# Optimization experiments

Hardware: AMD Instinct MI355X
Metric: run time of the kernel (lower is better)

## Reference

```python
import jax, jax.numpy as jnp
import numpy as np

# ---- Cl(4,1) algebra tables (metric: e1..e4 square to +1, e5 to -1) ----
_METRIC = [1.0, 1.0, 1.0, 1.0, -1.0]

def _popcount(x):
    return bin(x).count('1')

def _gp_blade(a, b):
    # geometric product of basis blades given as bitmasks -> (result_mask, sign)
    s = 1.0
    aa = a >> 1
    swaps = 0
    while aa:
        swaps += _popcount(aa & b)
        aa >>= 1
    if swaps & 1:
        s = -s
    for i in range(5):
        if (a & b) & (1 << i):
            s *= _METRIC[i]
    return a ^ b, s

def _build_gp_map():
    # lane ordering: blades sorted by (grade, bitmask) -> lane 0 scalar, 1..5 vectors, ...
    masks = sorted(range(32), key=lambda m: (_popcount(m), m))
    idx = {m: i for i, m in enumerate(masks)}
    gp = np.zeros((32, 32, 32), dtype=np.float32)
    for a in range(32):
        for b in range(32):
            r, s = _gp_blade(masks[a], masks[b])
            gp[a, b, idx[r]] = s
    return gp

_GP_NP = _build_gp_map()
# signature: scalar part of blade*blade (metric sign per lane)
_SIG_NP = np.array([_GP_NP[k, k, 0] for k in range(32)], dtype=np.float32)

N_HEADS = 8
EPS = 1e-6

def normalize_cl41(x):
    # normalize each 32-lane multivector to unit Euclidean magnitude
    n = jnp.sqrt(jnp.sum(x * x, axis=-1, keepdims=True) + EPS)
    return x / n

def versor_linear(x, w, gp):
    # x: (B,S,I,32), w: (O,I,32), gp: (32,32,32)
    w_op = jnp.einsum('oij,jlk->oilk', w, gp)          # (O,I,32,32)
    out = jnp.einsum('bsil,oilk->bsok', x, w_op)       # (B,S,O,32)
    return normalize_cl41(out)

def setup_inputs() -> dict:
    key = jax.random.key(0)
    ks = jax.random.split(key, 5)
    B, S, D = 2, 2048, 64
    std = 1.0 / (D * 32) ** 0.5
    x = jax.random.normal(ks[0], (B, S, D, 32), dtype=jnp.float32)
    wq = jax.random.normal(ks[1], (D, D, 32), dtype=jnp.float32) * std
    wk = jax.random.normal(ks[2], (D, D, 32), dtype=jnp.float32) * std
    wv = jax.random.normal(ks[3], (D, D, 32), dtype=jnp.float32) * std
    wo = jax.random.normal(ks[4], (D, D, 32), dtype=jnp.float32) * std
    return {'x': x, 'wq': wq, 'wk': wk, 'wv': wv, 'wo': wo}

def reference(x, wq, wk, wv, wo):
    gp = jnp.asarray(_GP_NP)
    sig = jnp.asarray(_SIG_NP)
    B, S, D, _ = x.shape
    H = N_HEADS
    hd = D // H
    def split_heads(t):
        return t.reshape(B, S, H, hd, 32).transpose(0, 2, 1, 3, 4)  # (B,H,S,hd,32)
    q = split_heads(versor_linear(x, wq, gp))
    k = split_heads(versor_linear(x, wk, gp))
    v = split_heads(versor_linear(x, wv, gp))
    q_flat = (q * sig).reshape(B, H, S, hd * 32)
    k_flat = k.reshape(B, H, S, hd * 32)
    score = jnp.einsum('bhqf,bhkf->bhqk', q_flat, k_flat) / (hd ** 0.5)
    attn = jax.nn.softmax(score, axis=-1)
    out = jnp.einsum('bhsi,bhidl->bhsdl', attn, v)      # (B,H,S,hd,32)
    out = out.transpose(0, 2, 1, 3, 4).reshape(B, S, D, 32)
    return versor_linear(out, wo, gp)
```

## Files before the change

### kernel.cpp

```cpp
#include <hip/hip_runtime.h>
#include <hip/hip_bf16.h>


typedef unsigned short u16;
typedef unsigned short u16x8 __attribute__((ext_vector_type(8)));
typedef unsigned short u16x4 __attribute__((ext_vector_type(4)));
typedef short          s16x8 __attribute__((ext_vector_type(8)));
typedef float          f32x4 __attribute__((ext_vector_type(4)));

#define B_DIM 2
#define S_DIM 2048
#define D_DIM 64
#define NH    8
#define HD    256
#define F_DIM 2048
#define TOK   4096

__constant__ int LANE_MASK[32] = {
    0,
    1, 2, 4, 8, 16,
    3, 5, 6, 9, 10, 12, 17, 18, 20, 24,
    7, 11, 13, 14, 19, 21, 22, 25, 26, 28,
    15, 23, 27, 29, 30,
    31};
__constant__ int MASK_LANE[32] = {
    0, 1, 2, 6, 3, 7, 8, 16, 4, 9, 10, 17, 11, 18, 19, 26,
    5, 12, 13, 20, 14, 21, 22, 27, 15, 23, 24, 28, 25, 29, 30, 31};

__device__ __forceinline__ float gp_sign(int a, int b) {
  int swaps = 0;
  int aa = a >> 1;
  while (aa) { swaps += __popc(aa & b); aa >>= 1; }
  float s = (swaps & 1) ? -1.0f : 1.0f;
  if (a & b & 16) s = -s;
  return s;
}

__device__ __forceinline__ u16 f2bf(float f) {
  unsigned u = __float_as_uint(f);
  u += 0x7fffu + ((u >> 16) & 1u);
  return (u16)(u >> 16);
}

__device__ __forceinline__ f32x4 mfma16(s16x8 a, s16x8 b, f32x4 c) {
  return __builtin_amdgcn_mfma_f32_16x16x32_bf16(a, b, c, 0, 0, 0);
}

__device__ __forceinline__ void gload16(const u16* g, u16* l) {
  __builtin_amdgcn_global_load_lds(
      (const __attribute__((address_space(1))) void*)g,
      (__attribute__((address_space(3))) void*)l, 16, 0, 0);
}

__global__ __launch_bounds__(256) void k_cast(const float* __restrict__ x,
                                              u16* __restrict__ xb) {
  int i = blockIdx.x * 256 + threadIdx.x;
  const float4* x4 = (const float4*)x;
  float4 a = x4[2 * i], b = x4[2 * i + 1];
  u16x8 r;
  r[0] = f2bf(a.x); r[1] = f2bf(a.y); r[2] = f2bf(a.z); r[3] = f2bf(a.w);
  r[4] = f2bf(b.x); r[5] = f2bf(b.y); r[6] = f2bf(b.z); r[7] = f2bf(b.w);
  *(u16x8*)&xb[8 * i] = r;
}

__global__ __launch_bounds__(256) void k_buildw(const float* __restrict__ w,
                                                u16* __restrict__ W) {
  __shared__ float wvals[32];
  __shared__ int   jt[1024];
  __shared__ float st[1024];
  const int o = blockIdx.x >> 6, i = blockIdx.x & 63;
  const int tid = threadIdx.x;
  for (int e = tid; e < 1024; e += 256) {
    int k = e >> 5, l = e & 31;
    int mk = LANE_MASK[k], ml = LANE_MASK[l];
    int mj = mk ^ ml;
    jt[e] = MASK_LANE[mj];
    st[e] = gp_sign(mj, ml);
  }
  if (tid < 32) wvals[tid] = w[(o * D_DIM + i) * 32 + tid];
  __syncthreads();
  for (int e = tid; e < 1024; e += 256) {
    int k = e >> 5, l = e & 31;
    size_t off = (size_t)(o * 32 + k) * F_DIM + i * 32 + l;
    W[off] = f2bf(st[e] * wvals[jt[e]]);
  }
}

__global__ __launch_bounds__(256) void k_gemm_qkv(const u16* __restrict__ A,
                                                  const u16* __restrict__ Wcat,
                                                  u16* __restrict__ Qb,
                                                  u16* __restrict__ Kb,
                                                  u16* __restrict__ Vt) {
  constexpr int K = F_DIM;
  __shared__ u16 As[128 * 64];
  __shared__ u16 Bs[128 * 64];
  const int tid = threadIdx.x;
  const int wid = tid >> 6, lane = tid & 63;
  const int region = blockIdx.x >> 4;
  const int col0 = (blockIdx.x & 15) * 128;
  const int row0 = blockIdx.y * 128;
  const u16* Bsrc = Wcat + (size_t)region * F_DIM * F_DIM;
  const int wm = (wid >> 1) * 64, wn = (wid & 1) * 64;
  const int lr = lane & 15, lk = (lane >> 4) * 8;
  const int srow = lane >> 3, scol = (lane & 7) * 8;

  f32x4 acc[4][4];
#pragma unroll
  for (int m = 0; m < 4; ++m)
#pragma unroll
    for (int n = 0; n < 4; ++n) acc[m][n] = (f32x4)0.0f;

  for (int k0 = 0; k0 < K; k0 += 64) {
#pragma unroll
    for (int it = 0; it < 4; ++it) {
      int c = it * 4 + wid;
      gload16(&A[(size_t)(row0 + c * 8 + srow) * K + k0 + scol], &As[c * 512]);
      gload16(&Bsrc[(size_t)(col0 + c * 8 + srow) * K + k0 + scol], &Bs[c * 512]);
    }
    __syncthreads();
#pragma unroll
    for (int ks = 0; ks < 64; ks += 32) {
      s16x8 af[4], bf[4];
#pragma unroll
      for (int m = 0; m < 4; ++m)
        af[m] = *(const s16x8*)&As[(wm + m * 16 + lr) * 64 + ks + lk];
#pragma unroll
      for (int n = 0; n < 4; ++n)
        bf[n] = *(const s16x8*)&Bs[(wn + n * 16 + lr) * 64 + ks + lk];
#pragma unroll
      for (int m = 0; m < 4; ++m)
#pragma unroll
        for (int n = 0; n < 4; ++n)
          acc[m][n] = mfma16(af[m], bf[n], acc[m][n]);
    }
    __syncthreads();
  }

  float sc0 = 1.0f, sc1 = 1.0f;
  if (region == 0) {
    const float qs = 0.35355339059327373f * 1.4426950408889634f;
    int m0 = LANE_MASK[lr], m1 = LANE_MASK[16 + lr];
    sc0 = gp_sign(m0, m0) * qs;
    sc1 = gp_sign(m1, m1) * qs;
  }
#pragma unroll
  for (int m = 0; m < 4; ++m) {
    int rowb = row0 + wm + m * 16 + (lane >> 4) * 4;
#pragma unroll
    for (int np = 0; np < 2; ++np) {
      int n0 = 2 * np, n1 = n0 + 1;
      int colb = col0 + wn + np * 32 + lr;
      f32x4 inv;
#pragma unroll
      for (int r = 0; r < 4; ++r) {
        float a0 = acc[m][n0][r], a1 = acc[m][n1][r];
        float s2 = a0 * a0 + a1 * a1;
        s2 += __shfl_xor(s2, 1);
        s2 += __shfl_xor(s2, 2);
        s2 += __shfl_xor(s2, 4);
        s2 += __shfl_xor(s2, 8);
        inv[r] = 1.0f / sqrtf(s2 + 1e-6f);
      }
      if (region == 2) {
        int bb = rowb >> 11, s0 = rowb & 2047;
        u16x4 p0, p1;
#pragma unroll
        for (int r = 0; r < 4; ++r) {
          p0[r] = f2bf(acc[m][n0][r] * inv[r]);
          p1[r] = f2bf(acc[m][n1][r] * inv[r]);
        }
        *(u16x4*)&Vt[((size_t)bb * F_DIM + colb) * S_DIM + s0] = p0;
        *(u16x4*)&Vt[((size_t)bb * F_DIM + colb + 16) * S_DIM + s0] = p1;
      } else {
        u16* dst = (region == 0) ? Qb : Kb;
#pragma unroll
        for (int r = 0; r < 4; ++r) {
          size_t o = (size_t)(rowb + r) * F_DIM + colb;
          dst[o]      = f2bf(acc[m][n0][r] * inv[r] * sc0);
          dst[o + 16] = f2bf(acc[m][n1][r] * inv[r] * sc1);
        }
      }
    }
  }
}

__global__ __launch_bounds__(256) void k_gemm_fin(const u16* __restrict__ A,
                                                  const u16* __restrict__ B,
                                                  float* __restrict__ outf) {
  constexpr int K = F_DIM, N = F_DIM;
  __shared__ u16 As[128 * 64];
  __shared__ u16 Bs[128 * 64];
  const int tid = threadIdx.x;
  const int wid = tid >> 6, lane = tid & 63;
  const int row0 = blockIdx.y * 128, col0 = blockIdx.x * 128;
  const int wm = (wid >> 1) * 64, wn = (wid & 1) * 64;
  const int lr = lane & 15, lk = (lane >> 4) * 8;
  const int srow = lane >> 3, scol = (lane & 7) * 8;

  f32x4 acc[4][4];
#pragma unroll
  for (int m = 0; m < 4; ++m)
#pragma unroll
    for (int n = 0; n < 4; ++n) acc[m][n] = (f32x4)0.0f;

  for (int k0 = 0; k0 < K; k0 += 64) {
#pragma unroll
    for (int it = 0; it < 4; ++it) {
      int c = it * 4 + wid;
      gload16(&A[(size_t)(row0 + c * 8 + srow) * K + k0 + scol], &As[c * 512]);
      gload16(&B[(size_t)(col0 + c * 8 + srow) * K + k0 + scol], &Bs[c * 512]);
    }
    __syncthreads();
#pragma unroll
    for (int ks = 0; ks < 64; ks += 32) {
      s16x8 af[4], bf[4];
#pragma unroll
      for (int m = 0; m < 4; ++m)
        af[m] = *(const s16x8*)&As[(wm + m * 16 + lr) * 64 + ks + lk];
#pragma unroll
      for (int n = 0; n < 4; ++n)
        bf[n] = *(const s16x8*)&Bs[(wn + n * 16 + lr) * 64 + ks + lk];
#pragma unroll
      for (int m = 0; m < 4; ++m)
#pragma unroll
        for (int n = 0; n < 4; ++n)
          acc[m][n] = mfma16(af[m], bf[n], acc[m][n]);
    }
    __syncthreads();
  }

#pragma unroll
  for (int m = 0; m < 4; ++m) {
    int rowb = row0 + wm + m * 16 + (lane >> 4) * 4;
#pragma unroll
    for (int np = 0; np < 2; ++np) {
      int n0 = 2 * np, n1 = n0 + 1;
      int colb = col0 + wn + np * 32 + lr;
#pragma unroll
      for (int r = 0; r < 4; ++r) {
        float a0 = acc[m][n0][r], a1 = acc[m][n1][r];
        float s2 = a0 * a0 + a1 * a1;
        s2 += __shfl_xor(s2, 1);
        s2 += __shfl_xor(s2, 2);
        s2 += __shfl_xor(s2, 4);
        s2 += __shfl_xor(s2, 8);
        float inv = 1.0f / sqrtf(s2 + 1e-6f);
        size_t o = (size_t)(rowb + r) * N + colb;
        outf[o]      = a0 * inv;
        outf[o + 16] = a1 * inv;
      }
    }
  }
}

__global__ __launch_bounds__(512, 2) void k_attn(const u16* __restrict__ qb,
                                                 const u16* __restrict__ kb,
                                                 const u16* __restrict__ vt,
                                                 u16* __restrict__ ao) {
  __shared__ u16 Kbuf[2][64 * 256];
  __shared__ u16 Vbuf[2][256 * 64];
  __shared__ u16 Ps[8][16][72];
  const int tid = threadIdx.x, wid = tid >> 6, lane = tid & 63;
  const int rid = (blockIdx.x & 7) * 32 + (blockIdx.x >> 3);
  const int qblk = rid & 15, bh = rid >> 4;
  const int b = bh >> 3, h = bh & 7;
  const int lr = lane & 15, hi = lane >> 4;
  const int lr7s = (lr & 7) << 3;
  const int q0 = qblk * 128 + wid * 16;

  const int krow_l = lane >> 5;
  const int kcolb  = (lane & 31) * 8;
  const int vrow_l = lane >> 3;
  const int vcol_l = ((lane & 7) * 8) ^ ((vrow_l & 7) << 3);

  u16x8 qf[8];
#pragma unroll
  for (int c = 0; c < 8; ++c)
    qf[c] = *(const u16x8*)&qb[(size_t)(b * S_DIM + q0 + lr) * F_DIM +
                               h * HD + c * 32 + hi * 8];

  float mrow[4], lacc[4];
#pragma unroll
  for (int r = 0; r < 4; ++r) { mrow[r] = -1e30f; lacc[r] = 0.0f; }
  f32x4 oacc[16];
#pragma unroll
  for (int d = 0; d < 16; ++d) oacc[d] = (f32x4)0.0f;

  const u16* kbase = kb + (size_t)b * S_DIM * F_DIM + h * HD;
  const u16* vbase = vt + ((size_t)b * F_DIM + h * HD) * S_DIM;

#pragma unroll
  for (int i = 0; i < 4; ++i) {
    int ck = wid * 4 + i;
    int kr = ck * 2 + krow_l;
    gload16(kbase + (size_t)kr * F_DIM + (kcolb ^ ((kr & 7) << 3)),
            &Kbuf[0][ck * 512]);
    int vr = ck * 8 + vrow_l;
    gload16(vbase + (size_t)vr * S_DIM + vcol_l, &Vbuf[0][ck * 512]);
  }
  __syncthreads();

  for (int t = 0; t < 32; ++t) {
    const int cur = t & 1;
    if (t < 31) {
      int kv1 = (t + 1) * 64;
#pragma unroll
      for (int i = 0; i < 4; ++i) {
        int ck = wid * 4 + i;
        int kr = ck * 2 + krow_l;
        gload16(kbase + (size_t)(kv1 + kr) * F_DIM + (kcolb ^ ((kr & 7) << 3)),
                &Kbuf[cur ^ 1][ck * 512]);
        int vr = ck * 8 + vrow_l;
        gload16(vbase + (size_t)vr * S_DIM + kv1 + vcol_l,
                &Vbuf[cur ^ 1][ck * 512]);
      }
    }

    f32x4 sacc[4];
#pragma unroll
    for (int n = 0; n < 4; ++n) sacc[n] = (f32x4)0.0f;
#pragma unroll
    for (int c = 0; c < 8; ++c) {
      s16x8 a = *(const s16x8*)&qf[c];
#pragma unroll
      for (int n = 0; n < 4; ++n) {
        s16x8 kf = *(const s16x8*)&Kbuf[cur][(n * 16 + lr) * 256 +
                                             ((c * 32 + hi * 8) ^ lr7s)];
        sacc[n] = mfma16(a, kf, sacc[n]);
      }
    }

    float pmax[4], need = 0.0f;
#pragma unroll
    for (int r = 0; r < 4; ++r) {
      float mx = fmaxf(fmaxf(sacc[0][r], sacc[1][r]),
                       fmaxf(sacc[2][r], sacc[3][r]));
      mx = fmaxf(mx, __shfl_xor(mx, 1));
      mx = fmaxf(mx, __shfl_xor(mx, 2));
      mx = fmaxf(mx, __shfl_xor(mx, 4));
      mx = fmaxf(mx, __shfl_xor(mx, 8));
      pmax[r] = mx;
      need = fmaxf(need, mx - mrow[r]);
    }
    if (!__all(need <= 8.0f)) {
#pragma unroll
      for (int r = 0; r < 4; ++r) {
        float mnew = fmaxf(mrow[r], pmax[r]);
        float alpha = exp2f(mrow[r] - mnew);
        mrow[r] = mnew;
        lacc[r] *= alpha;
#pragma unroll
        for (int d = 0; d < 16; ++d) oacc[d][r] *= alpha;
      }
    }
#pragma unroll
    for (int n = 0; n < 4; ++n)
#pragma unroll
      for (int r = 0; r < 4; ++r) {
        float p = exp2f(sacc[n][r] - mrow[r]);
        lacc[r] += p;
        Ps[wid][hi * 4 + r][n * 16 + lr] = f2bf(p);
      }

#pragma unroll
    for (int ks = 0; ks < 2; ++ks) {
      s16x8 pf = *(const s16x8*)&Ps[wid][lr][ks * 32 + hi * 8];
#pragma unroll
      for (int d0 = 0; d0 < 16; ++d0) {
        s16x8 vf = *(const s16x8*)&Vbuf[cur][(d0 * 16 + lr) * 64 +
                                             ((ks * 32 + hi * 8) ^ lr7s)];
        oacc[d0] = mfma16(pf, vf, oacc[d0]);
      }
    }
    __syncthreads();
  }

#pragma unroll
  for (int r = 0; r < 4; ++r) {
    float s = lacc[r];
    s += __shfl_xor(s, 1);
    s += __shfl_xor(s, 2);
    s += __shfl_xor(s, 4);
    s += __shfl_xor(s, 8);
    float inv = 1.0f / s;
    int row = q0 + hi * 4 + r;
#pragma unroll
    for (int d0 = 0; d0 < 16; ++d0)
      ao[(size_t)(b * S_DIM + row) * F_DIM + h * HD + d0 * 16 + lr] =
          f2bf(oacc[d0][r] * inv);
  }
}

extern "C" void kernel_launch(void* const* d_in, const int* in_sizes, int n_in,
                              void* d_out, int out_size, void* d_ws, size_t ws_size,
                              hipStream_t stream) {
  const float* x  = (const float*)d_in[0];
  const float* wq = (const float*)d_in[1];
  const float* wk = (const float*)d_in[2];
  const float* wv = (const float*)d_in[3];
  const float* wo = (const float*)d_in[4];

  char* ws = (char*)d_ws;
  const size_t SZ_XB = (size_t)TOK * F_DIM * sizeof(u16);
  const size_t SZ_W  = (size_t)F_DIM * F_DIM * sizeof(u16);
  u16* Xb   = (u16*)(ws);
  u16* Wcat = (u16*)(ws + SZ_XB);
  u16* Qb   = (u16*)(ws + SZ_XB + 3 * SZ_W);
  u16* Kb   = Qb + (size_t)TOK * F_DIM;
  u16* Vt   = (u16*)d_out;
  u16* Ao   = Xb;

  const int bw_blocks = D_DIM * D_DIM;

  k_cast<<<TOK * F_DIM / (256 * 8), 256, 0, stream>>>(x, Xb);

  k_buildw<<<bw_blocks, 256, 0, stream>>>(wq, Wcat);
  k_buildw<<<bw_blocks, 256, 0, stream>>>(wk, Wcat + (size_t)F_DIM * F_DIM);
  k_buildw<<<bw_blocks, 256, 0, stream>>>(wv, Wcat + 2 * (size_t)F_DIM * F_DIM);

  k_gemm_qkv<<<dim3(48, 32), 256, 0, stream>>>(Xb, Wcat, Qb, Kb, Vt);

  k_attn<<<B_DIM * NH * (S_DIM / 128), 512, 0, stream>>>(Qb, Kb, Vt, Ao);

  k_buildw<<<bw_blocks, 256, 0, stream>>>(wo, Wcat);
  k_gemm_fin<<<dim3(16, 32), 256, 0, stream>>>(Ao, Wcat, (float*)d_out);
}
```

Measured before the change: 443.3 us.

## Double-buffer LDS tiles in GEMMs and fuse weight-expansion launches

Both bf16 GEMM kernels now use two LDS buffers per operand. The next K-tile's global-to-LDS loads are issued before computing on the current tile, so memory latency overlaps the MFMA work. The four separate weight-expansion launches become one kernel that writes all four expanded matrices, with the output weights in their own workspace slot instead of being rebuilt after attention. The cost is double the LDS per GEMM block, which lowers occupancy, plus an extra weight matrix of workspace.

```diff
diff --git a/kernel.cpp b/kernel.cpp
--- a/kernel.cpp
+++ b/kernel.cpp
@@ -63,13 +63,17 @@
   *(u16x8*)&xb[8 * i] = r;
 }
 
-__global__ __launch_bounds__(256) void k_buildw(const float* __restrict__ w,
-                                                u16* __restrict__ W) {
-  __shared__ float wvals[32];
+__global__ __launch_bounds__(256) void k_buildw4(const float* __restrict__ wq,
+                                                 const float* __restrict__ wk,
+                                                 const float* __restrict__ wv,
+                                                 const float* __restrict__ wo,
+                                                 u16* __restrict__ W) {
+  __shared__ float wvals[4][32];
   __shared__ int   jt[1024];
   __shared__ float st[1024];
   const int o = blockIdx.x >> 6, i = blockIdx.x & 63;
   const int tid = threadIdx.x;
+  constexpr size_t WSZ = (size_t)F_DIM * F_DIM;
   for (int e = tid; e < 1024; e += 256) {
     int k = e >> 5, l = e & 31;
     int mk = LANE_MASK[k], ml = LANE_MASK[l];
@@ -77,12 +81,23 @@
     jt[e] = MASK_LANE[mj];
     st[e] = gp_sign(mj, ml);
   }
-  if (tid < 32) wvals[tid] = w[(o * D_DIM + i) * 32 + tid];
+  if (tid < 32) {
+    int base = (o * D_DIM + i) * 32 + tid;
+    wvals[0][tid] = wq[base];
+    wvals[1][tid] = wk[base];
+    wvals[2][tid] = wv[base];
+    wvals[3][tid] = wo[base];
+  }
   __syncthreads();
   for (int e = tid; e < 1024; e += 256) {
     int k = e >> 5, l = e & 31;
     size_t off = (size_t)(o * 32 + k) * F_DIM + i * 32 + l;
-    W[off] = f2bf(st[e] * wvals[jt[e]]);
+    float s = st[e];
+    int   j = jt[e];
+    W[off]           = f2bf(s * wvals[0][j]);
+    W[off + WSZ]     = f2bf(s * wvals[1][j]);
+    W[off + 2 * WSZ] = f2bf(s * wvals[2][j]);
+    W[off + 3 * WSZ] = f2bf(s * wvals[3][j]);
   }
 }
 
@@ -92,8 +107,8 @@
                                                   u16* __restrict__ Kb,
                                                   u16* __restrict__ Vt) {
   constexpr int K = F_DIM;
-  __shared__ u16 As[128 * 64];
-  __shared__ u16 Bs[128 * 64];
+  __shared__ u16 As[2][128 * 64];
+  __shared__ u16 Bs[2][128 * 64];
   const int tid = threadIdx.x;
   const int wid = tid >> 6, lane = tid & 63;
   const int region = blockIdx.x >> 4;
@@ -110,23 +125,36 @@
 #pragma unroll
     for (int n = 0; n < 4; ++n) acc[m][n] = (f32x4)0.0f;
 
-  for (int k0 = 0; k0 < K; k0 += 64) {
-#pragma unroll
-    for (int it = 0; it < 4; ++it) {
-      int c = it * 4 + wid;
-      gload16(&A[(size_t)(row0 + c * 8 + srow) * K + k0 + scol], &As[c * 512]);
-      gload16(&Bsrc[(size_t)(col0 + c * 8 + srow) * K + k0 + scol], &Bs[c * 512]);
-    }
-    __syncthreads();
+#pragma unroll
+  for (int it = 0; it < 4; ++it) {
+    int c = it * 4 + wid;
+    gload16(&A[(size_t)(row0 + c * 8 + srow) * K + scol], &As[0][c * 512]);
+    gload16(&Bsrc[(size_t)(col0 + c * 8 + srow) * K + scol], &Bs[0][c * 512]);
+  }
+  __syncthreads();
+
+  for (int kt = 0; kt < K / 64; ++kt) {
+    const int cur = kt & 1;
+    if (kt < K / 64 - 1) {
+      int k1 = (kt + 1) * 64;
+#pragma unroll
+      for (int it = 0; it < 4; ++it) {
+        int c = it * 4 + wid;
+        gload16(&A[(size_t)(row0 + c * 8 + srow) * K + k1 + scol],
+                &As[cur ^ 1][c * 512]);
+        gload16(&Bsrc[(size_t)(col0 + c * 8 + srow) * K + k1 + scol],
+                &Bs[cur ^ 1][c * 512]);
+      }
+    }
 #pragma unroll
     for (int ks = 0; ks < 64; ks += 32) {
       s16x8 af[4], bf[4];
 #pragma unroll
       for (int m = 0; m < 4; ++m)
-        af[m] = *(const s16x8*)&As[(wm + m * 16 + lr) * 64 + ks + lk];
+        af[m] = *(const s16x8*)&As[cur][(wm + m * 16 + lr) * 64 + ks + lk];
 #pragma unroll
       for (int n = 0; n < 4; ++n)
-        bf[n] = *(const s16x8*)&Bs[(wn + n * 16 + lr) * 64 + ks + lk];
+        bf[n] = *(const s16x8*)&Bs[cur][(wn + n * 16 + lr) * 64 + ks + lk];
 #pragma unroll
       for (int m = 0; m < 4; ++m)
 #pragma unroll
@@ -188,8 +216,8 @@
                                                   const u16* __restrict__ B,
                                                   float* __restrict__ outf) {
   constexpr int K = F_DIM, N = F_DIM;
-  __shared__ u16 As[128 * 64];
-  __shared__ u16 Bs[128 * 64];
+  __shared__ u16 As[2][128 * 64];
+  __shared__ u16 Bs[2][128 * 64];
   const int tid = threadIdx.x;
   const int wid = tid >> 6, lane = tid & 63;
   const int row0 = blockIdx.y * 128, col0 = blockIdx.x * 128;
@@ -203,23 +231,36 @@
 #pragma unroll
     for (int n = 0; n < 4; ++n) acc[m][n] = (f32x4)0.0f;
 
-  for (int k0 = 0; k0 < K; k0 += 64) {
-#pragma unroll
-    for (int it = 0; it < 4; ++it) {
-      int c = it * 4 + wid;
-      gload16(&A[(size_t)(row0 + c * 8 + srow) * K + k0 + scol], &As[c * 512]);
-      gload16(&B[(size_t)(col0 + c * 8 + srow) * K + k0 + scol], &Bs[c * 512]);
-    }
-    __syncthreads();
+#pragma unroll
+  for (int it = 0; it < 4; ++it) {
+    int c = it * 4 + wid;
+    gload16(&A[(size_t)(row0 + c * 8 + srow) * K + scol], &As[0][c * 512]);
+    gload16(&B[(size_t)(col0 + c * 8 + srow) * K + scol], &Bs[0][c * 512]);
+  }
+  __syncthreads();
+
+  for (int kt = 0; kt < K / 64; ++kt) {
+    const int cur = kt & 1;
+    if (kt < K / 64 - 1) {
+      int k1 = (kt + 1) * 64;
+#pragma unroll
+      for (int it = 0; it < 4; ++it) {
+        int c = it * 4 + wid;
+        gload16(&A[(size_t)(row0 + c * 8 + srow) * K + k1 + scol],
+                &As[cur ^ 1][c * 512]);
+        gload16(&B[(size_t)(col0 + c * 8 + srow) * K + k1 + scol],
+                &Bs[cur ^ 1][c * 512]);
+      }
+    }
 #pragma unroll
     for (int ks = 0; ks < 64; ks += 32) {
       s16x8 af[4], bf[4];
 #pragma unroll
       for (int m = 0; m < 4; ++m)
-        af[m] = *(const s16x8*)&As[(wm + m * 16 + lr) * 64 + ks + lk];
+        af[m] = *(const s16x8*)&As[cur][(wm + m * 16 + lr) * 64 + ks + lk];
 #pragma unroll
       for (int n = 0; n < 4; ++n)
-        bf[n] = *(const s16x8*)&Bs[(wn + n * 16 + lr) * 64 + ks + lk];
+        bf[n] = *(const s16x8*)&Bs[cur][(wn + n * 16 + lr) * 64 + ks + lk];
 #pragma unroll
       for (int m = 0; m < 4; ++m)
 #pragma unroll
@@ -405,23 +446,19 @@
   const size_t SZ_W  = (size_t)F_DIM * F_DIM * sizeof(u16);
   u16* Xb   = (u16*)(ws);
   u16* Wcat = (u16*)(ws + SZ_XB);
-  u16* Qb   = (u16*)(ws + SZ_XB + 3 * SZ_W);
+  u16* Qb   = (u16*)(ws + SZ_XB + 4 * SZ_W);
   u16* Kb   = Qb + (size_t)TOK * F_DIM;
   u16* Vt   = (u16*)d_out;
   u16* Ao   = Xb;
 
-  const int bw_blocks = D_DIM * D_DIM;
-
   k_cast<<<TOK * F_DIM / (256 * 8), 256, 0, stream>>>(x, Xb);
 
-  k_buildw<<<bw_blocks, 256, 0, stream>>>(wq, Wcat);
-  k_buildw<<<bw_blocks, 256, 0, stream>>>(wk, Wcat + (size_t)F_DIM * F_DIM);
-  k_buildw<<<bw_blocks, 256, 0, stream>>>(wv, Wcat + 2 * (size_t)F_DIM * F_DIM);
+  k_buildw4<<<D_DIM * D_DIM, 256, 0, stream>>>(wq, wk, wv, wo, Wcat);
 
   k_gemm_qkv<<<dim3(48, 32), 256, 0, stream>>>(Xb, Wcat, Qb, Kb, Vt);
 
   k_attn<<<B_DIM * NH * (S_DIM / 128), 512, 0, stream>>>(Qb, Kb, Vt, Ao);
 
-  k_buildw<<<bw_blocks, 256, 0, stream>>>(wo, Wcat);
-  k_gemm_fin<<<dim3(16, 32), 256, 0, stream>>>(Ao, Wcat, (float*)d_out);
-}
+  k_gemm_fin<<<dim3(16, 32), 256, 0, stream>>>(Ao, Wcat + 3 * (size_t)F_DIM * F_DIM,
+                                               (float*)d_out);
+}
```

Result: slower. 462.2 us (+4.3%).
